# Performance work log

Measured on AMD Instinct MI355X. Metric: run time of the kernel, lower is better.

Reference implementation:

```python
import jax, jax.numpy as jnp
import numpy as np

# ---- module hyperparameters (init_kwargs) ----
N = 32            # orthogonal matrix size
N_STAGES = 3      # number of scattering stages
SPARSITY = 3      # sparsity of generated FIR filters
GAIN_PER_SAMPLE = 0.9999
PULSE_SIZE = 1


def _make_shifts():
    """Faithful replica of get_random_shifts(N, sparsity_vect, pulse_size)."""
    rng = np.random.default_rng(0)
    sv = np.ones(N_STAGES)
    sv[0] = SPARSITY
    shifts = np.zeros((N_STAGES, N), dtype=np.int64)
    ps = float(PULSE_SIZE)
    for k in range(N_STAGES):
        temp = np.floor(sv[k] * (np.arange(N) + rng.random(N) * 0.99))
        shifts[k] = (temp * ps).astype(np.int64)
        ps = ps * N * sv[k]
    return shifts


def _delay_roll(V, s, row_axis):
    """shift_matrix: zero-pad the time axis so the max delay fits, then delay
    slice i along the last axis by s[i] samples (torch.roll with enough padding
    == pure delay). row_axis=0 -> 'left' (per-row), row_axis=1 -> 'right' (per-col).
    Generic inputs keep every tap occupied, so order == L-1 (matches the torch
    nonzero-based bookkeeping for random data)."""
    Nr, Nc, L = V.shape
    s = np.asarray(s).astype(np.int64)
    add = int(s.max())  # required_space.max() - L + 1 with order = L-1
    newL = L + add
    V = jnp.pad(V, ((0, 0), (0, 0), (0, add)))
    idx = (np.arange(newL)[None, :] - s[:, None]) % newL  # (N, newL) circular-roll gather
    if row_axis == 0:
        idx = jnp.broadcast_to(jnp.asarray(idx)[:, None, :], (Nr, Nc, newL))
    else:
        idx = jnp.broadcast_to(jnp.asarray(idx)[None, :, :], (Nr, Nc, newL))
    return jnp.take_along_axis(V, idx, axis=2)


def setup_inputs() -> dict:
    key = jax.random.key(0)
    U = jax.random.normal(key, (N_STAGES + 1, N, N), dtype=jnp.float32)
    shifts = jnp.asarray(_make_shifts(), dtype=jnp.int32)
    m_L = jnp.zeros((N,), dtype=jnp.int32)
    m_R = jnp.zeros((N,), dtype=jnp.int32)
    return {"U": U, "shifts": shifts, "m_L": m_L, "m_R": m_R}


def reference(U, shifts, m_L, m_R):
    # U: [K, N, N].  torch permutes to (N,N,K); V = U[:,:,0] == U[0], R stage k == U[k].
    shifts_np = np.asarray(shifts)
    K = U.shape[0]
    V = U[0][:, :, None]  # (N, N, 1) polynomial matrix
    g0 = jnp.asarray(GAIN_PER_SAMPLE, jnp.float32)
    for k in range(1, K):
        g = g0 ** shifts[k - 1].astype(jnp.float32)  # diag homogeneous attenuation
        R = U[k] * g[None, :]                        # U_k @ diag(g**shift)
        V = _delay_roll(V, shifts_np[k - 1], row_axis=0)   # left shift (per-row delay)
        # poly_matrix_conv with a length-1 polynomial R == per-tap matmul:
        # C[r,c,t] = sum_i R[r,i] * V[i,c,t]
        V = jnp.einsum('ri,ict->rct', R, V)
    V = _delay_roll(V, np.asarray(m_L), row_axis=0)  # final left shift m_{K+1}
    V = _delay_roll(V, np.asarray(m_R), row_axis=1)  # final right shift m_0
    return jnp.transpose(V, (2, 0, 1))  # (T, N, N)
```

## Files before the change

### kernel.cpp

```cpp
#include <hip/hip_runtime.h>


#define NN 32
#define LN_G -1.0000500033334732e-4f

typedef float fx4 __attribute__((ext_vector_type(4)));

__device__ __forceinline__ float tap_val(int tb, int r, int c,
                                         const float* __restrict__ sU,
                                         const int* __restrict__ inv) {
    if (tb < 0) return 0.0f;
    unsigned ut = (unsigned)tb;
    unsigned i2 = ut / 3072u;
    if (i2 >= 32u) return 0.0f;
    unsigned rem = ut - i2 * 3072u;
    unsigned i1 = rem / 96u;
    unsigned rem2 = rem - i1 * 96u;
    int i0 = inv[rem2];
    if (i0 < 0) return 0.0f;
    float gain = __expf((float)tb * LN_G);
    float f = sU[1 * NN * NN + i1 * NN + i0]
            * sU[2 * NN * NN + i2 * NN + i1]
            * sU[3 * NN * NN + r * NN + i2]
            * gain;
    return f * sU[i0 * NN + c];
}

__global__ __launch_bounds__(256) void scatter_fused_kernel(
    const float* __restrict__ U,
    const int*   __restrict__ shifts,
    const int*   __restrict__ mL,
    const int*   __restrict__ mR,
    float*       __restrict__ out,
    int T)
{
    __shared__ float sU[4 * NN * NN];
    __shared__ int inv[96];
    __shared__ int smL[NN], smR[NN];

    const int tid = threadIdx.x;
    if (tid < 96) inv[tid] = -1;
    __syncthreads();
    if (tid < NN) {
        int s1 = shifts[tid];
        if (s1 >= 0 && s1 < 96) inv[s1] = tid;
        smL[tid] = mL[tid];
        smR[tid] = mR[tid];
    }
    for (int k = tid; k < 4 * NN * NN; k += 256) sU[k] = U[k];
    __syncthreads();

    const int total4 = T * 256;
    const int stride = gridDim.x * 256;
    fx4* __restrict__ out4 = (fx4*)out;

    for (int idx = blockIdx.x * 256 + tid; idx < total4; idx += stride) {
        const int t = idx >> 8;
        const int pos = (idx & 255) * 4;
        const int r = pos >> 5;
        const int c = pos & 31;

        const int mlr = smL[r];
        const int m0 = smR[c], m1 = smR[c + 1], m2 = smR[c + 2], m3 = smR[c + 3];

        fx4 v;
        if (m0 == m1 && m1 == m2 && m2 == m3) {
            const int tb = t - mlr - m0;
            v = (fx4)0.0f;
            if (tb >= 0) {
                unsigned ut = (unsigned)tb;
                unsigned i2 = ut / 3072u;
                if (i2 < 32u) {
                    unsigned rem = ut - i2 * 3072u;
                    unsigned i1 = rem / 96u;
                    unsigned rem2 = rem - i1 * 96u;
                    int i0 = inv[rem2];
                    if (i0 >= 0) {
                        float gain = __expf((float)tb * LN_G);
                        float f = sU[1 * NN * NN + i1 * NN + i0]
                                * sU[2 * NN * NN + i2 * NN + i1]
                                * sU[3 * NN * NN + r * NN + i2]
                                * gain;
                        const fx4 u0 = ((const fx4*)(sU + i0 * NN))[c >> 2];
                        v = f * u0;
                    }
                }
            }
        } else {
            v.x = tap_val(t - mlr - m0, r, c + 0, sU, inv);
            v.y = tap_val(t - mlr - m1, r, c + 1, sU, inv);
            v.z = tap_val(t - mlr - m2, r, c + 2, sU, inv);
            v.w = tap_val(t - mlr - m3, r, c + 3, sU, inv);
        }
        __builtin_nontemporal_store(v, &out4[idx]);
    }
}

extern "C" void kernel_launch(void* const* d_in, const int* in_sizes, int n_in,
                              void* d_out, int out_size, void* d_ws, size_t ws_size,
                              hipStream_t stream) {
    const float* U      = (const float*)d_in[0];
    const int*   shifts = (const int*)d_in[1];
    const int*   mL     = (const int*)d_in[2];
    const int*   mR     = (const int*)d_in[3];
    float* out = (float*)d_out;

    const int T = out_size / (NN * NN);

    scatter_fused_kernel<<<dim3(2048), dim3(256), 0, stream>>>(
        U, shifts, mL, mR, out, T);
}
```

Before: 89.71 us.

## Assign one time step per wavefront and hoist shared tap decode

Each wavefront now handles one whole time slice of 32x32 outputs, so the tap-index decode, inv lookup and exp gain are computed once per wave instead of once per 4-element chunk. A block-wide uniformity check of the m_L/m_R shifts selects a fast path that reads a transposed U3 copy from shared memory. This cuts redundant integer division and shared loads per store. The cost is extra shared-memory setup and one more barrier per block. The kernel stays bound by output writes, so the gain may be small.

```diff
diff --git a/kernel.cpp b/kernel.cpp
--- a/kernel.cpp
+++ b/kernel.cpp
@@ -26,7 +26,7 @@
     return f * sU[i0 * NN + c];
 }
 
-__global__ __launch_bounds__(256) void scatter_fused_kernel(
+__global__ __launch_bounds__(256) void scatter_tile_kernel(
     const float* __restrict__ U,
     const int*   __restrict__ shifts,
     const int*   __restrict__ mL,
@@ -35,8 +35,10 @@
     int T)
 {
     __shared__ float sU[4 * NN * NN];
+    __shared__ float sU3T[NN * NN];
     __shared__ int inv[96];
     __shared__ int smL[NN], smR[NN];
+    __shared__ int sUniform, smL0, smR0;
 
     const int tid = threadIdx.x;
     if (tid < 96) inv[tid] = -1;
@@ -48,25 +50,38 @@
         smR[tid] = mR[tid];
     }
     for (int k = tid; k < 4 * NN * NN; k += 256) sU[k] = U[k];
+    for (int k = tid; k < NN * NN; k += 256) {
+        sU3T[(k & 31) * NN + (k >> 5)] = U[3 * NN * NN + k];
+    }
+    __syncthreads();
+    if (tid == 0) {
+        int uL = 1, uR = 1;
+        int a = smL[0], b = smR[0];
+        for (int i = 1; i < NN; ++i) {
+            uL &= (smL[i] == a);
+            uR &= (smR[i] == b);
+        }
+        sUniform = uL & uR;
+        smL0 = a;
+        smR0 = b;
+    }
     __syncthreads();
 
-    const int total4 = T * 256;
-    const int stride = gridDim.x * 256;
+    const int wave = tid >> 6;
+    const int lane = tid & 63;
+    const int nwaves = gridDim.x * 4;
+    const int uniform = sUniform;
+    const int mL0 = smL0, mR0 = smR0;
+
     fx4* __restrict__ out4 = (fx4*)out;
 
-    for (int idx = blockIdx.x * 256 + tid; idx < total4; idx += stride) {
-        const int t = idx >> 8;
-        const int pos = (idx & 255) * 4;
-        const int r = pos >> 5;
-        const int c = pos & 31;
-
-        const int mlr = smL[r];
-        const int m0 = smR[c], m1 = smR[c + 1], m2 = smR[c + 2], m3 = smR[c + 3];
-
-        fx4 v;
-        if (m0 == m1 && m1 == m2 && m2 == m3) {
-            const int tb = t - mlr - m0;
-            v = (fx4)0.0f;
+    for (int t = blockIdx.x * 4 + wave; t < T; t += nwaves) {
+        const size_t tbase = (size_t)t * 256;
+        if (uniform) {
+            const int tb = t - mL0 - mR0;
+            int i0 = 0, i2s = 0;
+            float fcom = 0.0f;
+            bool tap = false;
             if (tb >= 0) {
                 unsigned ut = (unsigned)tb;
                 unsigned i2 = ut / 3072u;
@@ -74,25 +89,47 @@
                     unsigned rem = ut - i2 * 3072u;
                     unsigned i1 = rem / 96u;
                     unsigned rem2 = rem - i1 * 96u;
-                    int i0 = inv[rem2];
-                    if (i0 >= 0) {
-                        float gain = __expf((float)tb * LN_G);
-                        float f = sU[1 * NN * NN + i1 * NN + i0]
-                                * sU[2 * NN * NN + i2 * NN + i1]
-                                * sU[3 * NN * NN + r * NN + i2]
-                                * gain;
-                        const fx4 u0 = ((const fx4*)(sU + i0 * NN))[c >> 2];
-                        v = f * u0;
+                    int ii0 = inv[rem2];
+                    if (ii0 >= 0) {
+                        tap = true;
+                        i0 = ii0;
+                        i2s = (int)i2;
+                        fcom = sU[1 * NN * NN + i1 * NN + ii0]
+                             * sU[2 * NN * NN + i2 * NN + i1]
+                             * __expf((float)tb * LN_G);
                     }
                 }
             }
+            if (tap) {
+                const fx4 u0v = ((const fx4*)(sU + i0 * NN))[lane & 7];
+                const int rl = lane >> 3;
+#pragma unroll
+                for (int j = 0; j < 4; ++j) {
+                    const float u3 = sU3T[i2s * NN + j * 8 + rl];
+                    const fx4 v = (fcom * u3) * u0v;
+                    __builtin_nontemporal_store(v, &out4[tbase + j * 64 + lane]);
+                }
+            } else {
+                const fx4 z = (fx4)0.0f;
+#pragma unroll
+                for (int j = 0; j < 4; ++j)
+                    __builtin_nontemporal_store(z, &out4[tbase + j * 64 + lane]);
+            }
         } else {
-            v.x = tap_val(t - mlr - m0, r, c + 0, sU, inv);
-            v.y = tap_val(t - mlr - m1, r, c + 1, sU, inv);
-            v.z = tap_val(t - mlr - m2, r, c + 2, sU, inv);
-            v.w = tap_val(t - mlr - m3, r, c + 3, sU, inv);
+#pragma unroll
+            for (int j = 0; j < 4; ++j) {
+                const int pos4 = j * 64 + lane;
+                const int r = pos4 >> 3;
+                const int c = (pos4 & 7) * 4;
+                const int mlr = smL[r];
+                fx4 v;
+                v.x = tap_val(t - mlr - smR[c + 0], r, c + 0, sU, inv);
+                v.y = tap_val(t - mlr - smR[c + 1], r, c + 1, sU, inv);
+                v.z = tap_val(t - mlr - smR[c + 2], r, c + 2, sU, inv);
+                v.w = tap_val(t - mlr - smR[c + 3], r, c + 3, sU, inv);
+                __builtin_nontemporal_store(v, &out4[tbase + pos4]);
+            }
         }
-        __builtin_nontemporal_store(v, &out4[idx]);
     }
 }
 
@@ -107,6 +144,6 @@
 
     const int T = out_size / (NN * NN);
 
-    scatter_fused_kernel<<<dim3(2048), dim3(256), 0, stream>>>(
+    scatter_tile_kernel<<<dim3(2048), dim3(256), 0, stream>>>(
         U, shifts, mL, mR, out, T);
 }
```

New measurement: 87.57 us. 2.4% less time.

## Map one wavefront per time step and skip shared-memory staging when shifts uniform

Applied to the files above, without the earlier changes.

Restructures the kernel so each 64-lane wavefront produces one full 32x32 time slice, with a 1024-thread block covering 16 time steps and a grid sized to T instead of a fixed grid-stride loop. When the final left and right shifts are uniform, the block skips staging U into shared memory and the syncthreads. It computes the tap once per wave, finding the stage-1 index with a ballot over shifts instead of an inverse table, and reads U directly from global memory. This is meant to remove the per-block 16KB LDS fill and the per-element divisions and index math in a kernel dominated by writes. The exchange is many more blocks, each re-reading small pieces of U from cache.

```diff
diff --git a/kernel.cpp b/kernel.cpp
--- a/kernel.cpp
+++ b/kernel.cpp
@@ -3,16 +3,16 @@
 
 #define NN 32
 #define LN_G -1.0000500033334732e-4f
+#define TMAX (NN * 3072)
 
 typedef float fx4 __attribute__((ext_vector_type(4)));
 
 __device__ __forceinline__ float tap_val(int tb, int r, int c,
                                          const float* __restrict__ sU,
                                          const int* __restrict__ inv) {
-    if (tb < 0) return 0.0f;
+    if (tb < 0 || tb >= TMAX) return 0.0f;
     unsigned ut = (unsigned)tb;
     unsigned i2 = ut / 3072u;
-    if (i2 >= 32u) return 0.0f;
     unsigned rem = ut - i2 * 3072u;
     unsigned i1 = rem / 96u;
     unsigned rem2 = rem - i1 * 96u;
@@ -26,7 +26,7 @@
     return f * sU[i0 * NN + c];
 }
 
-__global__ __launch_bounds__(256) void scatter_fused_kernel(
+__global__ __launch_bounds__(1024) void scat_wavetile_kernel(
     const float* __restrict__ U,
     const int*   __restrict__ shifts,
     const int*   __restrict__ mL,
@@ -34,65 +34,85 @@
     float*       __restrict__ out,
     int T)
 {
+    __shared__ int inv[96];
     __shared__ float sU[4 * NN * NN];
-    __shared__ int inv[96];
-    __shared__ int smL[NN], smR[NN];
 
-    const int tid = threadIdx.x;
+    const int tid  = threadIdx.x;
+    const int wave = tid >> 6;
+    const int lane = tid & 63;
+    const int l5   = lane & 31;
+
+    const int t = blockIdx.x * 16 + wave;
+
+    const int s1l = shifts[l5];
+    const int mll = mL[l5];
+    const int mrl = mR[l5];
+    const int mL0 = __shfl(mll, 0);
+    const int mR0 = __shfl(mrl, 0);
+    const bool uniform = __all(mll == mL0) && __all(mrl == mR0);
+
+    fx4* __restrict__ out4 = (fx4*)out;
+
+    if (uniform) {
+        if (t >= T) return;
+        const size_t tb4 = (size_t)t * 256;
+        const int tb = t - mL0 - mR0;
+        const int rl = lane >> 3;
+        const int cb = lane & 7;
+
+        fx4 v0, v1, v2, v3;
+        bool tap = false;
+        if (tb >= 0 && tb < TMAX) {
+            const int rem2 = tb % 96;
+            const unsigned long long bal = __ballot(s1l == rem2);
+            if (bal) {
+                tap = true;
+                const int i0 = __ffsll((long long)bal) - 1;
+                const int q  = tb / 96;
+                const int i1 = q & 31;
+                const int i2 = q >> 5;
+                const float fcom = U[1 * NN * NN + i1 * NN + i0]
+                                 * U[2 * NN * NN + i2 * NN + i1]
+                                 * __expf((float)tb * LN_G);
+                const fx4 u0v = ((const fx4*)(U + i0 * NN))[cb];
+                const float u30 = U[3 * NN * NN + (0 * 8 + rl) * NN + i2];
+                const float u31 = U[3 * NN * NN + (1 * 8 + rl) * NN + i2];
+                const float u32_ = U[3 * NN * NN + (2 * 8 + rl) * NN + i2];
+                const float u33 = U[3 * NN * NN + (3 * 8 + rl) * NN + i2];
+                v0 = (fcom * u30) * u0v;
+                v1 = (fcom * u31) * u0v;
+                v2 = (fcom * u32_) * u0v;
+                v3 = (fcom * u33) * u0v;
+            }
+        }
+        if (!tap) { v0 = v1 = v2 = v3 = (fx4)0.0f; }
+        __builtin_nontemporal_store(v0, &out4[tb4 + 0 * 64 + lane]);
+        __builtin_nontemporal_store(v1, &out4[tb4 + 1 * 64 + lane]);
+        __builtin_nontemporal_store(v2, &out4[tb4 + 2 * 64 + lane]);
+        __builtin_nontemporal_store(v3, &out4[tb4 + 3 * 64 + lane]);
+        return;
+    }
+
     if (tid < 96) inv[tid] = -1;
     __syncthreads();
-    if (tid < NN) {
-        int s1 = shifts[tid];
-        if (s1 >= 0 && s1 < 96) inv[s1] = tid;
-        smL[tid] = mL[tid];
-        smR[tid] = mR[tid];
-    }
-    for (int k = tid; k < 4 * NN * NN; k += 256) sU[k] = U[k];
+    if (tid < 32 && s1l >= 0 && s1l < 96) inv[s1l] = tid;
+    for (int k = tid; k < 4 * NN * NN; k += 1024) sU[k] = U[k];
     __syncthreads();
+    if (t >= T) return;
 
-    const int total4 = T * 256;
-    const int stride = gridDim.x * 256;
-    fx4* __restrict__ out4 = (fx4*)out;
-
-    for (int idx = blockIdx.x * 256 + tid; idx < total4; idx += stride) {
-        const int t = idx >> 8;
-        const int pos = (idx & 255) * 4;
-        const int r = pos >> 5;
-        const int c = pos & 31;
-
-        const int mlr = smL[r];
-        const int m0 = smR[c], m1 = smR[c + 1], m2 = smR[c + 2], m3 = smR[c + 3];
-
+    const size_t tb4 = (size_t)t * 256;
+#pragma unroll
+    for (int j = 0; j < 4; ++j) {
+        const int pos4 = j * 64 + lane;
+        const int r = pos4 >> 3;
+        const int c = (pos4 & 7) * 4;
+        const int mlr = __shfl(mll, r);
         fx4 v;
-        if (m0 == m1 && m1 == m2 && m2 == m3) {
-            const int tb = t - mlr - m0;
-            v = (fx4)0.0f;
-            if (tb >= 0) {
-                unsigned ut = (unsigned)tb;
-                unsigned i2 = ut / 3072u;
-                if (i2 < 32u) {
-                    unsigned rem = ut - i2 * 3072u;
-                    unsigned i1 = rem / 96u;
-                    unsigned rem2 = rem - i1 * 96u;
-                    int i0 = inv[rem2];
-                    if (i0 >= 0) {
-                        float gain = __expf((float)tb * LN_G);
-                        float f = sU[1 * NN * NN + i1 * NN + i0]
-                                * sU[2 * NN * NN + i2 * NN + i1]
-                                * sU[3 * NN * NN + r * NN + i2]
-                                * gain;
-                        const fx4 u0 = ((const fx4*)(sU + i0 * NN))[c >> 2];
-                        v = f * u0;
-                    }
-                }
-            }
-        } else {
-            v.x = tap_val(t - mlr - m0, r, c + 0, sU, inv);
-            v.y = tap_val(t - mlr - m1, r, c + 1, sU, inv);
-            v.z = tap_val(t - mlr - m2, r, c + 2, sU, inv);
-            v.w = tap_val(t - mlr - m3, r, c + 3, sU, inv);
-        }
-        __builtin_nontemporal_store(v, &out4[idx]);
+        v.x = tap_val(t - mlr - __shfl(mrl, c + 0), r, c + 0, sU, inv);
+        v.y = tap_val(t - mlr - __shfl(mrl, c + 1), r, c + 1, sU, inv);
+        v.z = tap_val(t - mlr - __shfl(mrl, c + 2), r, c + 2, sU, inv);
+        v.w = tap_val(t - mlr - __shfl(mrl, c + 3), r, c + 3, sU, inv);
+        __builtin_nontemporal_store(v, &out4[tb4 + pos4]);
     }
 }
 
@@ -106,7 +126,8 @@
     float* out = (float*)d_out;
 
     const int T = out_size / (NN * NN);
+    const int blocks = (T + 15) / 16;
 
-    scatter_fused_kernel<<<dim3(2048), dim3(256), 0, stream>>>(
+    scat_wavetile_kernel<<<dim3(blocks), dim3(1024), 0, stream>>>(
         U, shifts, mL, mR, out, T);
 }
```

After: 83.11 us. -7.4%, faster.
